# Optimization experiments

Hardware: AMD Instinct MI355X
Metric: run time of the kernel (lower is better)

## Reference

```python
import jax, jax.numpy as jnp
import numpy as np

HID = 1024

def setup_inputs() -> dict:
    key = jax.random.key(0)
    k1, k2, k3, k4, k5 = jax.random.split(key, 5)
    B, S, H = 16, 2048, HID
    queries = jax.random.normal(k1, (B, H), dtype=jnp.float32)
    keys = jax.random.normal(k2, (B, S, H), dtype=jnp.float32)
    values = jax.random.normal(k3, (B, S, H), dtype=jnp.float32)
    # additive_attention params: Linear(2H->H), ReLU, Linear(H->1)
    s1 = 1.0 / np.sqrt(2 * H)
    s2 = 1.0 / np.sqrt(H)
    W1 = jax.random.uniform(k4, (2 * H, H), dtype=jnp.float32, minval=-s1, maxval=s1)
    b1 = jnp.zeros((H,), dtype=jnp.float32)
    W2 = jax.random.uniform(k5, (H, 1), dtype=jnp.float32, minval=-s2, maxval=s2)
    b2 = jnp.zeros((1,), dtype=jnp.float32)
    return {"queries": queries, "keys": keys, "values": values,
            "W1": W1, "b1": b1, "W2": W2, "b2": b2}

def reference(queries, keys, values, W1, b1, W2, b2):
    B, S, H = keys.shape
    # concat expanded query with keys along feature dim: [B,S,2H]
    q_exp = jnp.broadcast_to(queries[:, None, :], (B, S, H))
    concat = jnp.concatenate([q_exp, keys], axis=-1)
    h = jax.nn.relu(jnp.einsum('bsf,fh->bsh', concat, W1) + b1)
    scores = jnp.einsum('bsh,ho->bso', h, W2) + b2          # [B,S,1]
    alphas = jax.nn.softmax(scores, axis=1)                  # softmax over seq
    # context = alphas^T @ values : [B,1,H]
    context = jnp.einsum('bso,bsh->boh', alphas, values)
    return (context, alphas)
```

## Files before the change

kernel.cpp:

```cpp
#include <hip/hip_runtime.h>

#define HID 1024
#define SEQ 2048
#define NB  16

typedef __attribute__((ext_vector_type(8))) short bf16x8;
typedef __attribute__((ext_vector_type(4))) float f32x4;

static __device__ __forceinline__ short f2bf(float f) {
    union { float f; unsigned u; } v; v.f = f;
    unsigned u = v.u + 0x7fffu + ((v.u >> 16) & 1u);
    return (short)(u >> 16);
}
static __device__ __forceinline__ unsigned pk2(float a, float b) {
    return (unsigned)(unsigned short)f2bf(a) | ((unsigned)(unsigned short)f2bf(b) << 16);
}
static __device__ __forceinline__ void glds16(const void* g, void* l) {
    __builtin_amdgcn_global_load_lds(
        (const __attribute__((address_space(1))) unsigned*)g,
        (__attribute__((address_space(3))) unsigned*)l, 16, 0, 0);
}

__global__ __launch_bounds__(256) void prep_all(const float* __restrict__ keys,
                                                short* __restrict__ kbf,
                                                const float* __restrict__ W1,
                                                const float* __restrict__ queries,
                                                const float* __restrict__ b1,
                                                short* __restrict__ w1t,
                                                float* __restrict__ qproj,
                                                float* __restrict__ scores,
                                                int nconv) {
    __shared__ float t[32][33];
    const int tid = threadIdx.x;
    int bw = blockIdx.x;
    if (bw < nconv) {
        const size_t i = ((size_t)bw * 256 + tid) * 8;
        const float4 a = *(const float4*)(keys + i);
        const float4 b = *(const float4*)(keys + i + 4);
        int4 o;
        o.x = (int)pk2(a.x, a.y); o.y = (int)pk2(a.z, a.w);
        o.z = (int)pk2(b.x, b.y); o.w = (int)pk2(b.z, b.w);
        *(int4*)(kbf + i) = o;
        return;
    }
    bw -= nconv;
    if (bw < 1024) {
        const int k0 = (bw & 31) * 32;
        const int n0 = (bw >> 5) * 32;
        const int tx = tid & 31, ty = tid >> 5;
#pragma unroll
        for (int i = 0; i < 32; i += 8)
            t[ty + i][tx] = W1[(size_t)(HID + k0 + ty + i) * HID + n0 + tx];
        __syncthreads();
#pragma unroll
        for (int i = 0; i < 32; i += 8)
            w1t[(size_t)(n0 + ty + i) * HID + k0 + tx] = f2bf(t[tx][ty + i]);
        return;
    }
    bw -= 1024;
    if (bw < 64) {
        const int u = bw * 256 + tid;
        const int b = u >> 10, n = u & 1023;
        const float* q = queries + b * HID;
        float acc = b1[n];
#pragma unroll 8
        for (int f = 0; f < HID; ++f)
            acc += q[f] * W1[(size_t)f * HID + n];
        qproj[u] = acc;
        return;
    }
    bw -= 64;
    {
        float4 z = {0.f, 0.f, 0.f, 0.f};
        *(float4*)(scores + (size_t)(bw * 256 + tid) * 4) = z;
    }
}

template<int PRE>
__global__ __launch_bounds__(256) void score_gemm128(const float* __restrict__ keys,
                                                     const short* __restrict__ kbf,
                                                     const short* __restrict__ w1t,
                                                     const float* __restrict__ qproj,
                                                     const float* __restrict__ W2,
                                                     float* __restrict__ scores) {
    __shared__ short As[128 * 32];
    __shared__ short Bs[128 * 32];

    const int tid  = threadIdx.x;
    const int lane = tid & 63;
    const int wave = tid >> 6;
    const int n0 = blockIdx.x * 128;
    const int m0 = blockIdx.y * 128;
    const int batch = m0 >> 11;
    const int wm = wave >> 1, wn = wave & 1;
    const int q = lane >> 4, c = lane & 15;

    const int lrow = lane >> 2;
    const int lk   = (lane & 3) * 8;

    f32x4 acc[4][4] = {};

    for (int k0 = 0; k0 < HID; k0 += 32) {
#pragma unroll
        for (int call = 0; call < 2; ++call) {
            const int rbase = (wave * 2 + call) * 16;
            glds16(w1t + (size_t)(n0 + rbase + lrow) * HID + k0 + lk,
                   &Bs[rbase * 32]);
        }
        if (PRE) {
#pragma unroll
            for (int call = 0; call < 2; ++call) {
                const int rbase = (wave * 2 + call) * 16;
                glds16(kbf + (size_t)(m0 + rbase + lrow) * HID + k0 + lk,
                       &As[rbase * 32]);
            }
        } else {
            const int r = tid >> 1, h = (tid & 1) * 16;
            const float* src = keys + (size_t)(m0 + r) * HID + k0 + h;
            const float4 v0 = *(const float4*)(src + 0);
            const float4 v1 = *(const float4*)(src + 4);
            const float4 v2 = *(const float4*)(src + 8);
            const float4 v3 = *(const float4*)(src + 12);
            int4 o0, o1;
            o0.x = (int)pk2(v0.x, v0.y); o0.y = (int)pk2(v0.z, v0.w);
            o0.z = (int)pk2(v1.x, v1.y); o0.w = (int)pk2(v1.z, v1.w);
            o1.x = (int)pk2(v2.x, v2.y); o1.y = (int)pk2(v2.z, v2.w);
            o1.z = (int)pk2(v3.x, v3.y); o1.w = (int)pk2(v3.z, v3.w);
            *(int4*)&As[r * 32 + h + 0] = o0;
            *(int4*)&As[r * 32 + h + 8] = o1;
        }
        __syncthreads();

        bf16x8 af[4], bf[4];
#pragma unroll
        for (int i = 0; i < 4; ++i)
            af[i] = *(const bf16x8*)&As[(wm * 64 + i * 16 + c) * 32 + q * 8];
#pragma unroll
        for (int i = 0; i < 4; ++i)
            bf[i] = *(const bf16x8*)&Bs[(wn * 64 + i * 16 + c) * 32 + q * 8];
#pragma unroll
        for (int mi = 0; mi < 4; ++mi)
#pragma unroll
            for (int ni = 0; ni < 4; ++ni)
                acc[mi][ni] = __builtin_amdgcn_mfma_f32_16x16x32_bf16(af[mi], bf[ni], acc[mi][ni], 0, 0, 0);
        __syncthreads();
    }

    const float* qp = qproj + batch * HID + n0 + wn * 64;
    const float* w2 = W2 + n0 + wn * 64;
    float psum[4][4] = {};
#pragma unroll
    for (int ni = 0; ni < 4; ++ni) {
        const float qv = qp[ni * 16 + c];
        const float wv = w2[ni * 16 + c];
#pragma unroll
        for (int mi = 0; mi < 4; ++mi)
#pragma unroll
            for (int r = 0; r < 4; ++r)
                psum[mi][r] += fmaxf(acc[mi][ni][r] + qv, 0.f) * wv;
    }
#pragma unroll
    for (int m = 1; m < 16; m <<= 1)
#pragma unroll
        for (int mi = 0; mi < 4; ++mi)
#pragma unroll
            for (int r = 0; r < 4; ++r)
                psum[mi][r] += __shfl_xor(psum[mi][r], m, 64);
    if (c == 0) {
#pragma unroll
        for (int mi = 0; mi < 4; ++mi) {
            const int row = m0 + wm * 64 + mi * 16 + q * 4;
#pragma unroll
            for (int r = 0; r < 4; ++r)
                atomicAdd(&scores[row + r], psum[mi][r]);
        }
    }
}

__global__ __launch_bounds__(256) void softmax_k(const float* __restrict__ scores,
                                                 float* __restrict__ alphas,
                                                 float* __restrict__ ctx) {
    __shared__ float red[256];
    const int b = blockIdx.x;
    const int tid = threadIdx.x;
    float4 z = {0.f, 0.f, 0.f, 0.f};
    *(float4*)(ctx + b * HID + tid * 4) = z;

    float loc[8];
    float mx = -1e30f;
#pragma unroll
    for (int i = 0; i < 8; ++i) {
        loc[i] = scores[b * SEQ + tid + i * 256];
        mx = fmaxf(mx, loc[i]);
    }
    red[tid] = mx; __syncthreads();
    for (int s = 128; s > 0; s >>= 1) {
        if (tid < s) red[tid] = fmaxf(red[tid], red[tid + s]);
        __syncthreads();
    }
    mx = red[0]; __syncthreads();
    float sum = 0.f;
#pragma unroll
    for (int i = 0; i < 8; ++i) { loc[i] = expf(loc[i] - mx); sum += loc[i]; }
    red[tid] = sum; __syncthreads();
    for (int s = 128; s > 0; s >>= 1) {
        if (tid < s) red[tid] += red[tid + s];
        __syncthreads();
    }
    const float inv = 1.0f / red[0];
#pragma unroll
    for (int i = 0; i < 8; ++i) alphas[b * SEQ + tid + i * 256] = loc[i] * inv;
}

__global__ __launch_bounds__(256) void context_k(const float* __restrict__ alphas,
                                                 const float* __restrict__ values,
                                                 float* __restrict__ context) {
    const int b = blockIdx.y;
    const int s0 = blockIdx.x * 64;
    const int col = threadIdx.x * 4;
    float4 acc = {0.f, 0.f, 0.f, 0.f};
    for (int i = 0; i < 64; ++i) {
        const int s = s0 + i;
        const float a = alphas[b * SEQ + s];
        const float4 v = *(const float4*)(values + (size_t)(b * SEQ + s) * HID + col);
        acc.x += a * v.x; acc.y += a * v.y; acc.z += a * v.z; acc.w += a * v.w;
    }
    float* cp = context + b * HID + col;
    atomicAdd(cp + 0, acc.x);
    atomicAdd(cp + 1, acc.y);
    atomicAdd(cp + 2, acc.z);
    atomicAdd(cp + 3, acc.w);
}

extern "C" void kernel_launch(void* const* d_in, const int* in_sizes, int n_in,
                              void* d_out, int out_size, void* d_ws, size_t ws_size,
                              hipStream_t stream) {
    const float* queries = (const float*)d_in[0];
    const float* keys    = (const float*)d_in[1];
    const float* values  = (const float*)d_in[2];
    const float* W1      = (const float*)d_in[3];
    const float* b1      = (const float*)d_in[4];
    const float* W2      = (const float*)d_in[5];

    float* out_ctx   = (float*)d_out;
    float* out_alpha = (float*)d_out + NB * HID;

    char* ws = (char*)d_ws;
    float* scores = (float*)ws;
    float* qproj  = (float*)(ws + 131072);
    short* w1t    = (short*)(ws + 196608);
    short* kbf    = (short*)(ws + 2293760);

    const size_t need_pre = 2293760ull + 67108864ull;
    const bool pre = ws_size >= need_pre;
    const int nconv = pre ? 16384 : 0;

    prep_all<<<nconv + 1024 + 64 + 32, 256, 0, stream>>>(
        keys, kbf, W1, queries, b1, w1t, qproj, scores, nconv);

    if (pre)
        score_gemm128<1><<<dim3(8, 256), 256, 0, stream>>>(keys, kbf, w1t, qproj, W2, scores);
    else
        score_gemm128<0><<<dim3(8, 256), 256, 0, stream>>>(keys, kbf, w1t, qproj, W2, scores);

    softmax_k<<<NB, 256, 0, stream>>>(scores, out_alpha, out_ctx);
    context_k<<<dim3(32, NB), 256, 0, stream>>>(out_alpha, values, out_ctx);
}
```

Measured before the change: 443.4 us.

## Split query projection into f-chunks with atomics and reorder prep blocks

Rewrites the query-projection part of the prep kernel. Each of 32 blocks now handles a 128-feature chunk for all 16 batches, keeping the queries in shared memory so every W1 load is reused across all batches, and combines partial sums with atomicAdd. The old path had 64 blocks each doing a serial 1024-step dot product per output. These long-running blocks, and the W1 transpose blocks, are placed ahead of the key-conversion blocks so they are scheduled first. Zeroing of scores and qproj moves to a hipMemsetAsync, which adds an extra launch and makes the float summation order nondeterministic.

```diff
diff --git a/kernel.cpp b/kernel.cpp
--- a/kernel.cpp
+++ b/kernel.cpp
@@ -28,11 +28,56 @@
                                                 const float* __restrict__ b1,
                                                 short* __restrict__ w1t,
                                                 float* __restrict__ qproj,
-                                                float* __restrict__ scores,
                                                 int nconv) {
-    __shared__ float t[32][33];
+    __shared__ float shmem[2048];
     const int tid = threadIdx.x;
     int bw = blockIdx.x;
+
+    if (bw < 32) {
+        const int f0 = (bw >> 2) * 128;
+        const int n0 = (bw & 3) * 256;
+#pragma unroll
+        for (int j = 0; j < 8; ++j) {
+            const int idx = tid * 8 + j;
+            const int b = idx >> 7, f = idx & 127;
+            shmem[idx] = queries[b * HID + f0 + f];
+        }
+        __syncthreads();
+        float acc[16];
+        const float bv = (bw >> 2 == 0) ? b1[n0 + tid] : 0.0f;
+#pragma unroll
+        for (int b = 0; b < 16; ++b) acc[b] = (b == 0) ? bv : 0.0f;
+        if (bw >> 2 == 0) {
+#pragma unroll
+            for (int b = 1; b < 16; ++b) acc[b] = bv;
+        }
+        for (int f = 0; f < 128; ++f) {
+            const float w = W1[(size_t)(f0 + f) * HID + n0 + tid];
+#pragma unroll
+            for (int b = 0; b < 16; ++b)
+                acc[b] += shmem[b * 128 + f] * w;
+        }
+#pragma unroll
+        for (int b = 0; b < 16; ++b)
+            atomicAdd(&qproj[b * HID + n0 + tid], acc[b]);
+        return;
+    }
+    bw -= 32;
+    if (bw < 1024) {
+        float (*t)[33] = (float(*)[33])shmem;
+        const int k0 = (bw & 31) * 32;
+        const int n0 = (bw >> 5) * 32;
+        const int tx = tid & 31, ty = tid >> 5;
+#pragma unroll
+        for (int i = 0; i < 32; i += 8)
+            t[ty + i][tx] = W1[(size_t)(HID + k0 + ty + i) * HID + n0 + tx];
+        __syncthreads();
+#pragma unroll
+        for (int i = 0; i < 32; i += 8)
+            w1t[(size_t)(n0 + ty + i) * HID + k0 + tx] = f2bf(t[tx][ty + i]);
+        return;
+    }
+    bw -= 1024;
     if (bw < nconv) {
         const size_t i = ((size_t)bw * 256 + tid) * 8;
         const float4 a = *(const float4*)(keys + i);
@@ -41,38 +86,6 @@
         o.x = (int)pk2(a.x, a.y); o.y = (int)pk2(a.z, a.w);
         o.z = (int)pk2(b.x, b.y); o.w = (int)pk2(b.z, b.w);
         *(int4*)(kbf + i) = o;
-        return;
-    }
-    bw -= nconv;
-    if (bw < 1024) {
-        const int k0 = (bw & 31) * 32;
-        const int n0 = (bw >> 5) * 32;
-        const int tx = tid & 31, ty = tid >> 5;
-#pragma unroll
-        for (int i = 0; i < 32; i += 8)
-            t[ty + i][tx] = W1[(size_t)(HID + k0 + ty + i) * HID + n0 + tx];
-        __syncthreads();
-#pragma unroll
-        for (int i = 0; i < 32; i += 8)
-            w1t[(size_t)(n0 + ty + i) * HID + k0 + tx] = f2bf(t[tx][ty + i]);
-        return;
-    }
-    bw -= 1024;
-    if (bw < 64) {
-        const int u = bw * 256 + tid;
-        const int b = u >> 10, n = u & 1023;
-        const float* q = queries + b * HID;
-        float acc = b1[n];
-#pragma unroll 8
-        for (int f = 0; f < HID; ++f)
-            acc += q[f] * W1[(size_t)f * HID + n];
-        qproj[u] = acc;
-        return;
-    }
-    bw -= 64;
-    {
-        float4 z = {0.f, 0.f, 0.f, 0.f};
-        *(float4*)(scores + (size_t)(bw * 256 + tid) * 4) = z;
     }
 }
 
@@ -255,8 +268,10 @@
     const bool pre = ws_size >= need_pre;
     const int nconv = pre ? 16384 : 0;
 
-    prep_all<<<nconv + 1024 + 64 + 32, 256, 0, stream>>>(
-        keys, kbf, W1, queries, b1, w1t, qproj, scores, nconv);
+    hipMemsetAsync(ws, 0, 196608, stream);
+
+    prep_all<<<32 + 1024 + nconv, 256, 0, stream>>>(
+        keys, kbf, W1, queries, b1, w1t, qproj, nconv);
 
     if (pre)
         score_gemm128<1><<<dim3(8, 256), 256, 0, stream>>>(keys, kbf, w1t, qproj, W2, scores);
```

Measured after the change: 383.0 us. -13.6%, faster.
